# Optimization experiments

Hardware: AMD Instinct MI355X
Metric: run time of the kernel (lower is better)

The kernel has to match this reference:

```python
import jax, jax.numpy as jnp
import numpy as np
import math

B, H, S, D = 2, 16, 2048, 64

def setup_inputs() -> dict:
    key = jax.random.key(0)
    kq, kk, kv = jax.random.split(key, 3)
    Q = jax.random.normal(kq, (B, H, S, D), dtype=jnp.float32)
    K = jax.random.normal(kk, (B, H, S, D), dtype=jnp.float32)
    V = jax.random.normal(kv, (B, H, S, D), dtype=jnp.float32)
    causal_mask = jnp.tril(jnp.ones((S, S), dtype=bool))
    return {"Q": Q, "K": K, "V": V, "causal_mask": causal_mask}

def reference(Q, K, V, causal_mask):
    d_k = K.shape[-1]
    scores = jnp.einsum('bhqd,bhkd->bhqk', Q, K) / math.sqrt(d_k)
    scores = jnp.where(causal_mask, scores, -jnp.inf)
    probs = jax.nn.softmax(scores, axis=-1)
    return jnp.einsum('bhqk,bhkd->bhqd', probs, V)
```

## Files before the change

kernel.cpp:

```cpp
#include <hip/hip_runtime.h>
#include <math.h>


constexpr int kS   = 2048;
constexpr int kD   = 64;
constexpr int kBH  = 32;
constexpr int kPad = 72;
constexpr int kBQ  = 128;
constexpr int kNQI = kS / kBQ;

typedef short short8 __attribute__((ext_vector_type(8)));
typedef float float4v __attribute__((ext_vector_type(4)));
typedef float float16v __attribute__((ext_vector_type(16)));
typedef unsigned short ushort4v __attribute__((ext_vector_type(4)));

static __device__ inline unsigned short f2bf(float f) {
  union { float f; unsigned u; } v; v.f = f;
  unsigned r = v.u + 0x7FFF + ((v.u >> 16) & 1);
  return (unsigned short)(r >> 16);
}

static __device__ inline short8 pack8(float4v a, float4v b) {
  short8 r;
  r[0] = (short)f2bf(a[0]); r[1] = (short)f2bf(a[1]);
  r[2] = (short)f2bf(a[2]); r[3] = (short)f2bf(a[3]);
  r[4] = (short)f2bf(b[0]); r[5] = (short)f2bf(b[1]);
  r[6] = (short)f2bf(b[2]); r[7] = (short)f2bf(b[3]);
  return r;
}

__global__ __launch_bounds__(256)
void prep_kernel(const float* __restrict__ K, const float* __restrict__ V,
                 unsigned short* __restrict__ Kb, unsigned short* __restrict__ VT) {
  __shared__ unsigned short tile[64 * kPad];
  const int tid = threadIdx.x;
  const int bh = blockIdx.y, st = blockIdx.x;
  const size_t ibase = (size_t)bh * kS * kD + (size_t)st * 64 * kD;
  const int r  = tid >> 2;
  const int c0 = (tid & 3) * 16;
  {
    const float* kp = K + ibase + (size_t)r * kD + c0;
    float4v a = *(const float4v*)(kp);
    float4v b = *(const float4v*)(kp + 4);
    float4v c = *(const float4v*)(kp + 8);
    float4v d = *(const float4v*)(kp + 12);
    unsigned short* dst = Kb + ibase + (size_t)r * kD + c0;
    *(short8*)dst       = pack8(a, b);
    *(short8*)(dst + 8) = pack8(c, d);
  }
  {
    const float* vp = V + ibase + (size_t)r * kD + c0;
    float4v a = *(const float4v*)(vp);
    float4v b = *(const float4v*)(vp + 4);
    float4v c = *(const float4v*)(vp + 8);
    float4v d = *(const float4v*)(vp + 12);
    unsigned short* t = &tile[r * kPad + c0];
    *(short8*)t       = pack8(a, b);
    *(short8*)(t + 8) = pack8(c, d);
  }
  __syncthreads();
  {
    const int dd = tid >> 2;
    const int s0 = (tid & 3) * 16;
    short8 w0, w1;
    #pragma unroll
    for (int i = 0; i < 8; ++i) {
      w0[i] = (short)tile[(s0 + i) * kPad + dd];
      w1[i] = (short)tile[(s0 + 8 + i) * kPad + dd];
    }
    unsigned short* vdst = VT + (size_t)bh * kD * kS + (size_t)dd * kS + st * 64 + s0;
    *(short8*)vdst       = w0;
    *(short8*)(vdst + 8) = w1;
  }
}

__global__ __launch_bounds__(256)
void fattn_kernel(const float* __restrict__ Q, const unsigned short* __restrict__ Kb,
                  const unsigned short* __restrict__ VT,
                  float* __restrict__ O0, float* __restrict__ O1,
                  float* __restrict__ Lp) {
  __shared__ __align__(16) unsigned short ldsK[64 * kPad];
  __shared__ __align__(16) unsigned short ldsVT[64 * kPad];
  __shared__ __align__(16) unsigned short ldsP[4 * 32 * kPad];

  const int tid  = threadIdx.x;
  const int wave = tid >> 6;
  const int lane = tid & 63;
  const int l31  = lane & 31;
  const int h    = lane >> 5;

  const int bh = blockIdx.y;
  const int bx = blockIdx.x;
  const int qi = (kNQI - 1) - (bx >> 1);
  const int z  = bx & 1;
  const int q0 = qi * kBQ;
  const int wq0 = q0 + wave * 32;

  const size_t base = (size_t)bh * kS * kD;

  short8 qf[4];
  {
    const float scl = 0.125f * 1.44269504089f;
    const float* qp = Q + base + (size_t)(wq0 + l31) * kD + h * 8;
    #pragma unroll
    for (int dk = 0; dk < 4; ++dk) {
      float4v a = *(const float4v*)(qp + dk * 16);
      float4v b = *(const float4v*)(qp + dk * 16 + 4);
      #pragma unroll
      for (int i = 0; i < 4; ++i) { a[i] *= scl; b[i] *= scl; }
      qf[dk] = pack8(a, b);
    }
  }

  float16v acc0, acc1;
  #pragma unroll
  for (int i = 0; i < 16; ++i) { acc0[i] = 0.f; acc1[i] = 0.f; }
  float lacc = 0.f;

  const int tBeg = z * (qi + 1);
  const int tEnd = tBeg + (qi + 1);

  const int srow = tid >> 2;
  const int sc0  = (tid & 3) * 16;
  const unsigned short* Kg = Kb + base + (size_t)(tBeg * 64 + srow) * kD + sc0;
  const unsigned short* Vg = VT + (size_t)bh * kD * kS + (size_t)srow * kS
                                + tBeg * 64 + sc0;

  short8 pk0 = *(const short8*)(Kg);
  short8 pk1 = *(const short8*)(Kg + 8);
  short8 pv0 = *(const short8*)(Vg);
  short8 pv1 = *(const short8*)(Vg + 8);

  unsigned short* pw = &ldsP[wave * 32 * kPad + l31 * kPad];

  for (int kt = tBeg; kt < tEnd; ++kt) {
    const int kb = kt * 64;
    __syncthreads();
    {
      unsigned short* kd = &ldsK[srow * kPad + sc0];
      *(short8*)kd       = pk0;
      *(short8*)(kd + 8) = pk1;
      unsigned short* vd = &ldsVT[srow * kPad + sc0];
      *(short8*)vd       = pv0;
      *(short8*)(vd + 8) = pv1;
    }
    __syncthreads();
    if (kt + 1 < tEnd) {
      Kg += 64 * kD;
      Vg += 64;
      pk0 = *(const short8*)(Kg);
      pk1 = *(const short8*)(Kg + 8);
      pv0 = *(const short8*)(Vg);
      pv1 = *(const short8*)(Vg + 8);
    }

    #pragma unroll
    for (int kt32 = 0; kt32 < 2; ++kt32) {
      const int ktb = kb + kt32 * 32;
      if (ktb > wq0 + 31) break;

      float16v s;
      #pragma unroll
      for (int i = 0; i < 16; ++i) s[i] = 0.f;
      const unsigned short* kro = &ldsK[(kt32 * 32 + l31) * kPad + h * 8];
      #pragma unroll
      for (int dk = 0; dk < 4; ++dk) {
        short8 kf = *(const short8*)(kro + dk * 16);
        s = __builtin_amdgcn_mfma_f32_32x32x16_bf16(kf, qf[dk], s, 0, 0, 0);
      }

      if (ktb + 31 > wq0) {
        const int qg = wq0 + l31;
        #pragma unroll
        for (int r = 0; r < 16; ++r) {
          const int kg = ktb + (r & 3) + 8 * (r >> 2) + 4 * h;
          if (kg > qg) s[r] = -1e30f;
        }
      }

      #pragma unroll
      for (int rb = 0; rb < 4; ++rb) {
        ushort4v w;
        #pragma unroll
        for (int i = 0; i < 4; ++i) {
          float p = __builtin_amdgcn_exp2f(s[rb * 4 + i]);
          lacc += p;
          w[i] = (unsigned short)(__float_as_uint(p) >> 16);
        }
        *(ushort4v*)(pw + kt32 * 32 + rb * 8 + 4 * h) = w;
      }

      #pragma unroll
      for (int kc2 = 0; kc2 < 2; ++kc2) {
        const int ko = kt32 * 32 + kc2 * 16;
        short8 pf  = *(const short8*)(pw + ko + h * 8);
        short8 vf0 = *(const short8*)(&ldsVT[l31 * kPad + ko + h * 8]);
        short8 vf1 = *(const short8*)(&ldsVT[(32 + l31) * kPad + ko + h * 8]);
        acc0 = __builtin_amdgcn_mfma_f32_32x32x16_bf16(pf, vf0, acc0, 0, 0, 0);
        acc1 = __builtin_amdgcn_mfma_f32_32x32x16_bf16(pf, vf1, acc1, 0, 0, 0);
      }
    }
  }

  lacc += __shfl_xor(lacc, 32);
  if (h == 0) Lp[(size_t)z * kBH * kS + (size_t)bh * kS + wq0 + l31] = lacc;

  float* Od = z ? O1 : O0;
  #pragma unroll
  for (int r = 0; r < 16; ++r) {
    const int row = (r & 3) + 8 * (r >> 2) + 4 * h;
    float* op = Od + base + (size_t)(wq0 + row) * kD + l31;
    op[0]  = acc0[r];
    op[32] = acc1[r];
  }
}

__global__ __launch_bounds__(256)
void combine_kernel(const float* __restrict__ O1, const float* __restrict__ Lp,
                    float* __restrict__ O) {
  const int idx4 = blockIdx.x * 256 + threadIdx.x;
  const int row  = idx4 >> 4;
  const float l  = Lp[row] + Lp[kBH * kS + row];
  const float inv = 1.f / l;
  float4v a = ((const float4v*)O)[idx4];
  float4v b = ((const float4v*)O1)[idx4];
  #pragma unroll
  for (int i = 0; i < 4; ++i) a[i] = (a[i] + b[i]) * inv;
  ((float4v*)O)[idx4] = a;
}

extern "C" void kernel_launch(void* const* d_in, const int* in_sizes, int n_in,
                              void* d_out, int out_size, void* d_ws, size_t ws_size,
                              hipStream_t stream) {
  const float* Q = (const float*)d_in[0];
  const float* K = (const float*)d_in[1];
  const float* V = (const float*)d_in[2];
  float* O = (float*)d_out;

  const size_t nKV = (size_t)kBH * kS * kD;
  unsigned short* Kb = (unsigned short*)d_ws;
  unsigned short* VT = Kb + nKV;
  float* O1 = (float*)(VT + nKV);
  float* Lp = O1 + nKV;

  dim3 gprep(kS / 64, kBH);
  prep_kernel<<<gprep, 256, 0, stream>>>(K, V, Kb, VT);
  dim3 grid(kNQI * 2, kBH);
  fattn_kernel<<<grid, 256, 0, stream>>>(Q, Kb, VT, O, O1, Lp);
  const int n4 = (int)(nKV / 4);
  combine_kernel<<<n4 / 256, 256, 0, stream>>>(O1, Lp, O);
}
```

Measured before the change: 149.8 us.

## Pair causal query tiles, split work four ways, async double-buffer K/V into LDS

The attention kernel now pairs query tile p with tile 15-p so every block covers a balanced 34 key tiles, split evenly across four partial-sum workers instead of two. K/V tiles are loaded with global_load_lds async copies into double-buffered, XOR-swizzled LDS, replacing the register-staged single buffer. The P matrix is passed to the PV MFMA through register shuffles instead of an LDS round trip. The combine kernel now reads four partial outputs, which adds workspace and memory traffic.

```diff
diff --git a/kernel.cpp b/kernel.cpp
--- a/kernel.cpp
+++ b/kernel.cpp
@@ -5,19 +5,18 @@
 constexpr int kS   = 2048;
 constexpr int kD   = 64;
 constexpr int kBH  = 32;
-constexpr int kPad = 72;
-constexpr int kBQ  = 128;
-constexpr int kNQI = kS / kBQ;
+constexpr int kPadP = 72;
 
 typedef short short8 __attribute__((ext_vector_type(8)));
 typedef float float4v __attribute__((ext_vector_type(4)));
 typedef float float16v __attribute__((ext_vector_type(16)));
-typedef unsigned short ushort4v __attribute__((ext_vector_type(4)));
-
-static __device__ inline unsigned short f2bf(float f) {
+typedef unsigned int u32;
+typedef unsigned short u16;
+
+static __device__ inline u16 f2bf(float f) {
   union { float f; unsigned u; } v; v.f = f;
   unsigned r = v.u + 0x7FFF + ((v.u >> 16) & 1);
-  return (unsigned short)(r >> 16);
+  return (u16)(r >> 16);
 }
 
 static __device__ inline short8 pack8(float4v a, float4v b) {
@@ -29,10 +28,16 @@
   return r;
 }
 
+static __device__ inline void async_cp16(const void* g, void* l) {
+  __builtin_amdgcn_global_load_lds(
+      (const __attribute__((address_space(1))) u32*)g,
+      (__attribute__((address_space(3))) u32*)l, 16, 0, 0);
+}
+
 __global__ __launch_bounds__(256)
 void prep_kernel(const float* __restrict__ K, const float* __restrict__ V,
-                 unsigned short* __restrict__ Kb, unsigned short* __restrict__ VT) {
-  __shared__ unsigned short tile[64 * kPad];
+                 u16* __restrict__ Kb, u16* __restrict__ VT) {
+  __shared__ u16 tile[64 * kPadP];
   const int tid = threadIdx.x;
   const int bh = blockIdx.y, st = blockIdx.x;
   const size_t ibase = (size_t)bh * kS * kD + (size_t)st * 64 * kD;
@@ -44,7 +49,7 @@
     float4v b = *(const float4v*)(kp + 4);
     float4v c = *(const float4v*)(kp + 8);
     float4v d = *(const float4v*)(kp + 12);
-    unsigned short* dst = Kb + ibase + (size_t)r * kD + c0;
+    u16* dst = Kb + ibase + (size_t)r * kD + c0;
     *(short8*)dst       = pack8(a, b);
     *(short8*)(dst + 8) = pack8(c, d);
   }
@@ -54,7 +59,7 @@
     float4v b = *(const float4v*)(vp + 4);
     float4v c = *(const float4v*)(vp + 8);
     float4v d = *(const float4v*)(vp + 12);
-    unsigned short* t = &tile[r * kPad + c0];
+    u16* t = &tile[r * kPadP + c0];
     *(short8*)t       = pack8(a, b);
     *(short8*)(t + 8) = pack8(c, d);
   }
@@ -65,23 +70,23 @@
     short8 w0, w1;
     #pragma unroll
     for (int i = 0; i < 8; ++i) {
-      w0[i] = (short)tile[(s0 + i) * kPad + dd];
-      w1[i] = (short)tile[(s0 + 8 + i) * kPad + dd];
-    }
-    unsigned short* vdst = VT + (size_t)bh * kD * kS + (size_t)dd * kS + st * 64 + s0;
+      w0[i] = (short)tile[(s0 + i) * kPadP + dd];
+      w1[i] = (short)tile[(s0 + 8 + i) * kPadP + dd];
+    }
+    u16* vdst = VT + (size_t)bh * kD * kS + (size_t)dd * kS + st * 64 + s0;
     *(short8*)vdst       = w0;
     *(short8*)(vdst + 8) = w1;
   }
 }
 
-__global__ __launch_bounds__(256)
-void fattn_kernel(const float* __restrict__ Q, const unsigned short* __restrict__ Kb,
-                  const unsigned short* __restrict__ VT,
+__global__ __launch_bounds__(256, 4)
+void fattn_kernel(const float* __restrict__ Q, const u16* __restrict__ Kb,
+                  const u16* __restrict__ VT,
                   float* __restrict__ O0, float* __restrict__ O1,
+                  float* __restrict__ O2, float* __restrict__ O3,
                   float* __restrict__ Lp) {
-  __shared__ __align__(16) unsigned short ldsK[64 * kPad];
-  __shared__ __align__(16) unsigned short ldsVT[64 * kPad];
-  __shared__ __align__(16) unsigned short ldsP[4 * 32 * kPad];
+  __shared__ __align__(16) u16 ldsK[2][4096];
+  __shared__ __align__(16) u16 ldsV[2][4096];
 
   const int tid  = threadIdx.x;
   const int wave = tid >> 6;
@@ -90,142 +95,164 @@
   const int h    = lane >> 5;
 
   const int bh = blockIdx.y;
-  const int bx = blockIdx.x;
-  const int qi = (kNQI - 1) - (bx >> 1);
-  const int z  = bx & 1;
-  const int q0 = qi * kBQ;
-  const int wq0 = q0 + wave * 32;
-
-  const size_t base = (size_t)bh * kS * kD;
-
-  short8 qf[4];
-  {
-    const float scl = 0.125f * 1.44269504089f;
-    const float* qp = Q + base + (size_t)(wq0 + l31) * kD + h * 8;
-    #pragma unroll
-    for (int dk = 0; dk < 4; ++dk) {
-      float4v a = *(const float4v*)(qp + dk * 16);
-      float4v b = *(const float4v*)(qp + dk * 16 + 4);
-      #pragma unroll
-      for (int i = 0; i < 4; ++i) { a[i] *= scl; b[i] *= scl; }
-      qf[dk] = pack8(a, b);
-    }
-  }
-
-  float16v acc0, acc1;
-  #pragma unroll
-  for (int i = 0; i < 16; ++i) { acc0[i] = 0.f; acc1[i] = 0.f; }
-  float lacc = 0.f;
-
-  const int tBeg = z * (qi + 1);
-  const int tEnd = tBeg + (qi + 1);
-
-  const int srow = tid >> 2;
-  const int sc0  = (tid & 3) * 16;
-  const unsigned short* Kg = Kb + base + (size_t)(tBeg * 64 + srow) * kD + sc0;
-  const unsigned short* Vg = VT + (size_t)bh * kD * kS + (size_t)srow * kS
-                                + tBeg * 64 + sc0;
-
-  short8 pk0 = *(const short8*)(Kg);
-  short8 pk1 = *(const short8*)(Kg + 8);
-  short8 pv0 = *(const short8*)(Vg);
-  short8 pv1 = *(const short8*)(Vg + 8);
-
-  unsigned short* pw = &ldsP[wave * 32 * kPad + l31 * kPad];
-
-  for (int kt = tBeg; kt < tEnd; ++kt) {
-    const int kb = kt * 64;
-    __syncthreads();
+  const int p  = blockIdx.x >> 2;
+  const int z  = blockIdx.x & 3;
+  const int qiA = p, qiB = 15 - p;
+  const int nA  = 2 * qiA + 2;
+
+  const size_t base  = (size_t)bh * kS * kD;
+  const size_t vbase = (size_t)bh * kD * kS;
+
+  const int lr  = lane >> 3;
+  const int cxl = (lane & 7) ^ lr;
+  const int offK0 = lr * 64   + cxl * 8;
+  const int offV0 = lr * 2048 + cxl * 8;
+  const unsigned hs16 = ((unsigned)(h ^ (l31 & 7))) * 16;
+
+  float* Od = (z == 0) ? O0 : (z == 1) ? O1 : (z == 2) ? O2 : O3;
+
+  const int cB = (34 * z) / 4;
+  const int cE = (34 * (z + 1)) / 4;
+
+  int par = 0;
+  for (int seg = 0; seg < 2; ++seg) {
+    const int qi = seg ? qiB : qiA;
+    int tb, te;
+    if (seg == 0) { tb = min(cB, nA); te = min(cE, nA); }
+    else          { tb = max(cB, nA) - nA; te = max(cE, nA) - nA; }
+    const int q0  = qi * 128;
+    const int wq0 = q0 + wave * 32;
+
+    short8 qf[4];
     {
-      unsigned short* kd = &ldsK[srow * kPad + sc0];
-      *(short8*)kd       = pk0;
-      *(short8*)(kd + 8) = pk1;
-      unsigned short* vd = &ldsVT[srow * kPad + sc0];
-      *(short8*)vd       = pv0;
-      *(short8*)(vd + 8) = pv1;
-    }
-    __syncthreads();
-    if (kt + 1 < tEnd) {
-      Kg += 64 * kD;
-      Vg += 64;
-      pk0 = *(const short8*)(Kg);
-      pk1 = *(const short8*)(Kg + 8);
-      pv0 = *(const short8*)(Vg);
-      pv1 = *(const short8*)(Vg + 8);
-    }
-
-    #pragma unroll
-    for (int kt32 = 0; kt32 < 2; ++kt32) {
-      const int ktb = kb + kt32 * 32;
-      if (ktb > wq0 + 31) break;
-
-      float16v s;
-      #pragma unroll
-      for (int i = 0; i < 16; ++i) s[i] = 0.f;
-      const unsigned short* kro = &ldsK[(kt32 * 32 + l31) * kPad + h * 8];
+      const float scl = 0.125f * 1.44269504089f;
+      const float* qp = Q + base + (size_t)(wq0 + l31) * kD + h * 8;
       #pragma unroll
       for (int dk = 0; dk < 4; ++dk) {
-        short8 kf = *(const short8*)(kro + dk * 16);
-        s = __builtin_amdgcn_mfma_f32_32x32x16_bf16(kf, qf[dk], s, 0, 0, 0);
+        float4v a = *(const float4v*)(qp + dk * 16);
+        float4v b = *(const float4v*)(qp + dk * 16 + 4);
+        #pragma unroll
+        for (int i = 0; i < 4; ++i) { a[i] *= scl; b[i] *= scl; }
+        qf[dk] = pack8(a, b);
       }
-
-      if (ktb + 31 > wq0) {
-        const int qg = wq0 + l31;
+    }
+
+    float16v acc0, acc1;
+    #pragma unroll
+    for (int i = 0; i < 16; ++i) { acc0[i] = 0.f; acc1[i] = 0.f; }
+    float lacc = 0.f;
+
+    if (tb < te) {
+      {
+        const u16* kg0 = Kb + base + (size_t)tb * 4096;
+        const u16* vg0 = VT + vbase + tb * 64;
+        const int b = par & 1;
         #pragma unroll
-        for (int r = 0; r < 16; ++r) {
-          const int kg = ktb + (r & 3) + 8 * (r >> 2) + 4 * h;
-          if (kg > qg) s[r] = -1e30f;
+        for (int j = 0; j < 2; ++j) {
+          const int g = wave + 4 * j;
+          async_cp16(kg0 + g * 512 + offK0,   &ldsK[b][g * 512]);
+          async_cp16(vg0 + (size_t)g * 16384 + offV0, &ldsV[b][g * 512]);
         }
       }
-
-      #pragma unroll
-      for (int rb = 0; rb < 4; ++rb) {
-        ushort4v w;
+      for (int t = tb; t < te; ++t, ++par) {
+        __syncthreads();
+        if (t + 1 < te) {
+          const u16* kg0 = Kb + base + (size_t)(t + 1) * 4096;
+          const u16* vg0 = VT + vbase + (t + 1) * 64;
+          const int b = (par + 1) & 1;
+          #pragma unroll
+          for (int j = 0; j < 2; ++j) {
+            const int g = wave + 4 * j;
+            async_cp16(kg0 + g * 512 + offK0,   &ldsK[b][g * 512]);
+            async_cp16(vg0 + (size_t)g * 16384 + offV0, &ldsV[b][g * 512]);
+          }
+        }
+        const char* KB = (const char*)ldsK[par & 1];
+        const char* VB = (const char*)ldsV[par & 1];
         #pragma unroll
-        for (int i = 0; i < 4; ++i) {
-          float p = __builtin_amdgcn_exp2f(s[rb * 4 + i]);
-          lacc += p;
-          w[i] = (unsigned short)(__float_as_uint(p) >> 16);
+        for (int kt32 = 0; kt32 < 2; ++kt32) {
+          const int ktb = t * 64 + kt32 * 32;
+          if (ktb > wq0 + 31) break;
+
+          float16v s;
+          #pragma unroll
+          for (int i = 0; i < 16; ++i) s[i] = 0.f;
+          const char* krow = KB + (kt32 * 32 + l31) * 128;
+          #pragma unroll
+          for (int dk = 0; dk < 4; ++dk) {
+            short8 kf = *(const short8*)(krow + (((unsigned)(dk * 32)) ^ hs16));
+            s = __builtin_amdgcn_mfma_f32_32x32x16_bf16(kf, qf[dk], s, 0, 0, 0);
+          }
+
+          if (ktb + 31 > wq0) {
+            const int qg = wq0 + l31;
+            #pragma unroll
+            for (int r = 0; r < 16; ++r) {
+              const int kg = ktb + (r & 3) + 8 * (r >> 2) + 4 * h;
+              if (kg > qg) s[r] = -1e30f;
+            }
+          }
+
+          u32 pk[8];
+          #pragma unroll
+          for (int g2 = 0; g2 < 4; ++g2) {
+            float p0 = __builtin_amdgcn_exp2f(s[4 * g2 + 0]);
+            float p1 = __builtin_amdgcn_exp2f(s[4 * g2 + 1]);
+            float p2 = __builtin_amdgcn_exp2f(s[4 * g2 + 2]);
+            float p3 = __builtin_amdgcn_exp2f(s[4 * g2 + 3]);
+            lacc += (p0 + p1) + (p2 + p3);
+            pk[2 * g2]     = (__float_as_uint(p0) >> 16) | (__float_as_uint(p1) & 0xFFFF0000u);
+            pk[2 * g2 + 1] = (__float_as_uint(p2) >> 16) | (__float_as_uint(p3) & 0xFFFF0000u);
+          }
+          u32 ek[8];
+          #pragma unroll
+          for (int i = 0; i < 8; ++i) ek[i] = (u32)__shfl_xor((int)pk[i], 32);
+
+          #pragma unroll
+          for (int c = 0; c < 2; ++c) {
+            const int ga = 4 * c, gb = 4 * c + 2;
+            union { u32 u[4]; short8 s8; } pf;
+            pf.u[0] = h ? ek[gb]     : pk[ga];
+            pf.u[1] = h ? ek[gb + 1] : pk[ga + 1];
+            pf.u[2] = h ? pk[gb]     : ek[ga];
+            pf.u[3] = h ? pk[gb + 1] : ek[ga + 1];
+            const unsigned coff = ((unsigned)((kt32 * 4 + 2 * c) * 16)) ^ hs16;
+            short8 vf0 = *(const short8*)(VB + l31 * 128 + coff);
+            short8 vf1 = *(const short8*)(VB + (32 + l31) * 128 + coff);
+            acc0 = __builtin_amdgcn_mfma_f32_32x32x16_bf16(pf.s8, vf0, acc0, 0, 0, 0);
+            acc1 = __builtin_amdgcn_mfma_f32_32x32x16_bf16(pf.s8, vf1, acc1, 0, 0, 0);
+          }
         }
-        *(ushort4v*)(pw + kt32 * 32 + rb * 8 + 4 * h) = w;
       }
-
-      #pragma unroll
-      for (int kc2 = 0; kc2 < 2; ++kc2) {
-        const int ko = kt32 * 32 + kc2 * 16;
-        short8 pf  = *(const short8*)(pw + ko + h * 8);
-        short8 vf0 = *(const short8*)(&ldsVT[l31 * kPad + ko + h * 8]);
-        short8 vf1 = *(const short8*)(&ldsVT[(32 + l31) * kPad + ko + h * 8]);
-        acc0 = __builtin_amdgcn_mfma_f32_32x32x16_bf16(pf, vf0, acc0, 0, 0, 0);
-        acc1 = __builtin_amdgcn_mfma_f32_32x32x16_bf16(pf, vf1, acc1, 0, 0, 0);
-      }
-    }
-  }
-
-  lacc += __shfl_xor(lacc, 32);
-  if (h == 0) Lp[(size_t)z * kBH * kS + (size_t)bh * kS + wq0 + l31] = lacc;
-
-  float* Od = z ? O1 : O0;
-  #pragma unroll
-  for (int r = 0; r < 16; ++r) {
-    const int row = (r & 3) + 8 * (r >> 2) + 4 * h;
-    float* op = Od + base + (size_t)(wq0 + row) * kD + l31;
-    op[0]  = acc0[r];
-    op[32] = acc1[r];
+    }
+
+    lacc += __shfl_xor(lacc, 32);
+    if (h == 0) Lp[(size_t)z * kBH * kS + (size_t)bh * kS + wq0 + l31] = lacc;
+    #pragma unroll
+    for (int r = 0; r < 16; ++r) {
+      const int row = (r & 3) + 8 * (r >> 2) + 4 * h;
+      float* op = Od + base + (size_t)(wq0 + row) * kD + l31;
+      op[0]  = acc0[r];
+      op[32] = acc1[r];
+    }
   }
 }
 
 __global__ __launch_bounds__(256)
-void combine_kernel(const float* __restrict__ O1, const float* __restrict__ Lp,
+void combine_kernel(const float* __restrict__ O1, const float* __restrict__ O2,
+                    const float* __restrict__ O3, const float* __restrict__ Lp,
                     float* __restrict__ O) {
   const int idx4 = blockIdx.x * 256 + threadIdx.x;
   const int row  = idx4 >> 4;
-  const float l  = Lp[row] + Lp[kBH * kS + row];
+  const int N = kBH * kS;
+  const float l = Lp[row] + Lp[N + row] + Lp[2 * N + row] + Lp[3 * N + row];
   const float inv = 1.f / l;
   float4v a = ((const float4v*)O)[idx4];
   float4v b = ((const float4v*)O1)[idx4];
+  float4v c = ((const float4v*)O2)[idx4];
+  float4v d = ((const float4v*)O3)[idx4];
   #pragma unroll
-  for (int i = 0; i < 4; ++i) a[i] = (a[i] + b[i]) * inv;
+  for (int i = 0; i < 4; ++i) a[i] = ((a[i] + b[i]) + (c[i] + d[i])) * inv;
   ((float4v*)O)[idx4] = a;
 }
 
@@ -238,15 +265,16 @@
   float* O = (float*)d_out;
 
   const size_t nKV = (size_t)kBH * kS * kD;
-  unsigned short* Kb = (unsigned short*)d_ws;
-  unsigned short* VT = Kb + nKV;
+  u16* Kb = (u16*)d_ws;
+  u16* VT = Kb + nKV;
   float* O1 = (float*)(VT + nKV);
-  float* Lp = O1 + nKV;
+  float* O2 = O1 + nKV;
+  float* O3 = O2 + nKV;
+  float* Lp = O3 + nKV;
 
   dim3 gprep(kS / 64, kBH);
   prep_kernel<<<gprep, 256, 0, stream>>>(K, V, Kb, VT);
-  dim3 grid(kNQI * 2, kBH);
-  fattn_kernel<<<grid, 256, 0, stream>>>(Q, Kb, VT, O, O1, Lp);
-  const int n4 = (int)(nKV / 4);
-  combine_kernel<<<n4 / 256, 256, 0, stream>>>(O1, Lp, O);
-}
+  dim3 grid(32, kBH);
+  fattn_kernel<<<grid, 256, 0, stream>>>(Q, Kb, VT, O, O1, O2, O3, Lp);
+  combine_kernel<<<(int)(nKV / 4 / 256), 256, 0, stream>>>(O1, O2, O3, Lp, O);
+}
```

After: 147.4 us. About the same (-1.6%).
